# Kernel tuning notes

Hardware: AMD Instinct MI355X
Metric: run time of the kernel (lower is better)

Reference implementation:

```python
import jax, jax.numpy as jnp
import numpy as np

NUM_QUBITS = 22
NUM_LAYERS = 4
DIM = 2 ** NUM_QUBITS


def _apply_1q(state, U, q):
    # state: flat [2^n]; apply 2x2 unitary U on wire q (wire 0 = most significant)
    s = state.reshape(2 ** q, 2, -1)
    return jnp.einsum('ab,ibj->iaj', U, s).reshape(-1)


def _apply_cnot_adj(state, q):
    # CNOT with control q, target q+1 (adjacent wires)
    s = state.reshape(2 ** q, 2, 2, -1)
    s = jnp.stack([s[:, 0], s[:, 1, ::-1]], axis=1)
    return s.reshape(-1)


def _rot_mats(theta_x, theta_y, theta_z):
    cx = jnp.cos(theta_x / 2).astype(jnp.complex64)
    sx = jnp.sin(theta_x / 2).astype(jnp.complex64)
    RX = jnp.stack([jnp.stack([cx, -1j * sx]), jnp.stack([-1j * sx, cx])])
    cy = jnp.cos(theta_y / 2).astype(jnp.complex64)
    sy = jnp.sin(theta_y / 2).astype(jnp.complex64)
    RY = jnp.stack([jnp.stack([cy, -sy]), jnp.stack([sy, cy])])
    tz = theta_z.astype(jnp.complex64)
    zero = jnp.zeros((), jnp.complex64)
    RZ = jnp.stack([jnp.stack([jnp.exp(-1j * tz / 2), zero]),
                    jnp.stack([zero, jnp.exp(1j * tz / 2)])])
    return RX, RY, RZ


def _circuit(params, state):
    for l in range(NUM_LAYERS):
        for q in range(NUM_QUBITS):
            RX, RY, RZ = _rot_mats(params[l, q, 0], params[l, q, 1], params[l, q, 2])
            state = _apply_1q(state, RX, q)
            state = _apply_1q(state, RY, q)
            state = _apply_1q(state, RZ, q)
        for q in range(NUM_QUBITS - 1):
            state = _apply_cnot_adj(state, q)
    # <Z_q> for each qubit
    probs = jnp.abs(state) ** 2
    expvals = []
    for q in range(NUM_QUBITS):
        p = probs.reshape(2 ** q, 2, -1)
        expvals.append(p[:, 0].sum() - p[:, 1].sum())
    return jnp.stack(expvals).astype(jnp.float32)


def setup_inputs() -> dict:
    key = jax.random.key(0)
    k1, k2, k3 = jax.random.split(key, 3)
    params = jax.random.normal(k1, (NUM_LAYERS, NUM_QUBITS, 3), dtype=jnp.float32)
    state_re = jax.random.normal(k2, (DIM,), dtype=jnp.float32)
    state_im = jax.random.normal(k3, (DIM,), dtype=jnp.float32)
    return {"params": params, "state_re": state_re, "state_im": state_im}


def reference(params, state_re, state_im):
    state = (state_re + 1j * state_im).astype(jnp.complex64)
    state = state / jnp.sqrt(jnp.sum(jnp.abs(state) ** 2))
    return _circuit(params, state)
```

## Files before the change

kernel.cpp:

```cpp
#include <hip/hip_runtime.h>
#include <math.h>

#define NQ 22
#define DIM (1u << NQ)

typedef float v2f __attribute__((ext_vector_type(2)));

__global__ void k_gates(const float* __restrict__ params, float* __restrict__ U) {
  int t = blockIdx.x * blockDim.x + threadIdx.x;
  if (t >= 88) return;
  const float* p = params + t * 3;
  double hx = 0.5 * (double)p[0], hy = 0.5 * (double)p[1], hz = 0.5 * (double)p[2];
  double cx = cos(hx), sx = sin(hx);
  double cy = cos(hy), sy = sin(hy);
  double cz = cos(hz), sz = sin(hz);
  double m00r = cy * cx, m00i = sy * sx;
  double m01r = -sy * cx, m01i = -cy * sx;
  double m10r = sy * cx, m10i = -cy * sx;
  double m11r = cy * cx, m11i = -sy * sx;
  float* o = U + t * 8;
  o[0] = (float)(cz * m00r + sz * m00i); o[1] = (float)(cz * m00i - sz * m00r);
  o[2] = (float)(cz * m01r + sz * m01i); o[3] = (float)(cz * m01i - sz * m01r);
  o[4] = (float)(cz * m10r - sz * m10i); o[5] = (float)(cz * m10i + sz * m10r);
  o[6] = (float)(cz * m11r - sz * m11i); o[7] = (float)(cz * m11i + sz * m11r);
}

template <int NP>
__device__ __forceinline__ void apply_bit0(v2f RE[NP], v2f IM[NP], const float* __restrict__ u) {
  float u0 = u[0], u1 = u[1], u2 = u[2], u3 = u[3], u4 = u[4], u5 = u[5], u6 = u[6], u7 = u[7];
#pragma unroll
  for (int k = 0; k < NP; ++k) {
    float a0r = RE[k].x, a0i = IM[k].x, a1r = RE[k].y, a1i = IM[k].y;
    float n0r = u0 * a0r - u1 * a0i + u2 * a1r - u3 * a1i;
    float n0i = u0 * a0i + u1 * a0r + u2 * a1i + u3 * a1r;
    float n1r = u4 * a0r - u5 * a0i + u6 * a1r - u7 * a1i;
    float n1i = u4 * a0i + u5 * a0r + u6 * a1i + u7 * a1r;
    RE[k].x = n0r; IM[k].x = n0i; RE[k].y = n1r; IM[k].y = n1i;
  }
}

template <int NP, int PB>
__device__ __forceinline__ void apply_bitP(v2f RE[NP], v2f IM[NP], const float* __restrict__ u) {
  float u0 = u[0], u1 = u[1], u2 = u[2], u3 = u[3], u4 = u[4], u5 = u[5], u6 = u[6], u7 = u[7];
#pragma unroll
  for (int m = 0; m < NP / 2; ++m) {
    int k0 = ((m >> PB) << (PB + 1)) | (m & ((1 << PB) - 1));
    int k1 = k0 | (1 << PB);
    v2f a0r = RE[k0], a0i = IM[k0], a1r = RE[k1], a1i = IM[k1];
    v2f n0r = u0 * a0r - u1 * a0i + u2 * a1r - u3 * a1i;
    v2f n0i = u0 * a0i + u1 * a0r + u2 * a1i + u3 * a1r;
    v2f n1r = u4 * a0r - u5 * a0i + u6 * a1r - u7 * a1i;
    v2f n1i = u4 * a0i + u5 * a0r + u6 * a1i + u7 * a1r;
    RE[k0] = n0r; IM[k0] = n0i; RE[k1] = n1r; IM[k1] = n1i;
  }
}

__device__ __forceinline__ void apply4p(v2f RE[8], v2f IM[8], const float* __restrict__ U,
                                        int l, int wtop) {
  const float* base = U + ((l * 22 + wtop) << 3);
  apply_bit0<8>(RE, IM, base);
  apply_bitP<8, 0>(RE, IM, base - 8);
  apply_bitP<8, 1>(RE, IM, base - 16);
  apply_bitP<8, 2>(RE, IM, base - 24);
}

__device__ __forceinline__ void apply5p(v2f RE[16], v2f IM[16], const float* __restrict__ U,
                                        int l, int wtop) {
  const float* base = U + ((l * 22 + wtop) << 3);
  apply_bit0<16>(RE, IM, base);
  apply_bitP<16, 0>(RE, IM, base - 8);
  apply_bitP<16, 1>(RE, IM, base - 16);
  apply_bitP<16, 2>(RE, IM, base - 24);
  apply_bitP<16, 3>(RE, IM, base - 32);
}

template <typename WI, typename RI>
__device__ __forceinline__ void xchgP(float2* lds2, v2f RE[8], v2f IM[8], WI wi, RI ri) {
  __syncthreads();
#pragma unroll
  for (int d = 0; d < 16; ++d) {
    float2 a;
    if (d & 1) a = make_float2(RE[d >> 1].y, IM[d >> 1].y);
    else       a = make_float2(RE[d >> 1].x, IM[d >> 1].x);
    lds2[wi(d)] = a;
  }
  __syncthreads();
#pragma unroll
  for (int d = 0; d < 16; ++d) {
    float2 a = lds2[ri(d)];
    if (d & 1) { RE[d >> 1].y = a.x; IM[d >> 1].y = a.y; }
    else       { RE[d >> 1].x = a.x; IM[d >> 1].x = a.y; }
  }
}

__global__ __launch_bounds__(256, 4) void k_passA(const float* __restrict__ srcRe,
                                                  const float* __restrict__ srcIm,
                                                  const float2* __restrict__ src2,
                                                  float2* __restrict__ dst,
                                                  const float* __restrict__ U,
                                                  int layer, int first) {
  __shared__ float2 lds2[4096];
  const int t = threadIdx.x;
  const unsigned base = ((unsigned)blockIdx.x << 12) | ((unsigned)t << 4);
  v2f RE[8], IM[8];
  if (first) {
    const float4* r4 = (const float4*)(srcRe + base);
    const float4* i4 = (const float4*)(srcIm + base);
#pragma unroll
    for (int k = 0; k < 4; ++k) {
      float4 r = r4[k], m = i4[k];
      RE[2 * k].x     = r.x; RE[2 * k].y     = r.y;
      IM[2 * k].x     = m.x; IM[2 * k].y     = m.y;
      RE[2 * k + 1].x = r.z; RE[2 * k + 1].y = r.w;
      IM[2 * k + 1].x = m.z; IM[2 * k + 1].y = m.w;
    }
  } else {
    const unsigned b = base >> 4;
    const unsigned W = (b ^ (b >> 1)) << 4;
    const float4* s4 = (const float4*)(src2 + W);
    v2f WR[8], WI[8];
#pragma unroll
    for (int k = 0; k < 8; ++k) {
      float4 x = s4[k];
      WR[k].x = x.x; WR[k].y = x.z;
      WI[k].x = x.y; WI[k].y = x.w;
    }
    if (b & 1) {
#pragma unroll
      for (int k = 0; k < 4; ++k) {
        v2f tr = WR[k]; WR[k] = WR[k + 4]; WR[k + 4] = tr;
        v2f ti = WI[k]; WI[k] = WI[k + 4]; WI[k + 4] = ti;
      }
    }
#pragma unroll
    for (int k = 0; k < 8; ++k) {
      const int s = (2 * k) ^ k;
      const int j = s >> 1;
      if (s & 1) {
        RE[k].x = WR[j].y; RE[k].y = WR[j].x;
        IM[k].x = WI[j].y; IM[k].y = WI[j].x;
      } else {
        RE[k] = WR[j]; IM[k] = WI[j];
      }
    }
  }
  auto wA = [&](int d) { unsigned j = ((unsigned)t << 4) | (unsigned)d; return (int)(j ^ (j >> 4)); };
  auto rB = [&](int d) { unsigned j = (((unsigned)t >> 4) << 8) | ((unsigned)d << 4) | ((unsigned)t & 15); return (int)(j ^ (j >> 4)); };
  auto rC = [&](int d) { unsigned j = ((unsigned)d << 8) | (unsigned)t; return (int)(j ^ (j >> 4)); };

  apply4p(RE, IM, U, layer, 21);
  xchgP(lds2, RE, IM, wA, rB);
  apply4p(RE, IM, U, layer, 17);
  xchgP(lds2, RE, IM, rB, rC);
  apply4p(RE, IM, U, layer, 13);
  xchgP(lds2, RE, IM, rC, wA);
  float4* o4 = (float4*)(dst + base);
#pragma unroll
  for (int k = 0; k < 8; ++k)
    o4[k] = make_float4(RE[k].x, IM[k].x, RE[k].y, IM[k].y);
}

__device__ __forceinline__ int pb_lds_idx(unsigned h, unsigned c) {
  unsigned e = (h << 4) | (c ^ ((h ^ (h >> 5)) & 15u));
  return (int)(e ^ (((h >> 5) & 1u) << 4));
}

__global__ __launch_bounds__(512, 2) void k_passB(const float2* __restrict__ src,
                                                  float2* __restrict__ dst,
                                                  const float* __restrict__ U,
                                                  int layer) {
  __shared__ float lds[16384];
  const int t = threadIdx.x;
  const unsigned c = (unsigned)(t & 15), u = (unsigned)(t >> 4);
  const unsigned lowbase = ((unsigned)blockIdx.x << 4) | c;
  v2f RE[16], IM[16];
#pragma unroll
  for (int d = 0; d < 32; ++d) {
    unsigned h = u | ((unsigned)d << 5);
    float2 a = src[(h << 12) | lowbase];
    if (d & 1) { RE[d >> 1].y = a.x; IM[d >> 1].y = a.y; }
    else       { RE[d >> 1].x = a.x; IM[d >> 1].x = a.y; }
  }
  apply5p(RE, IM, U, layer, 4);
  __syncthreads();
#pragma unroll
  for (int d = 0; d < 32; ++d) {
    unsigned h = u | ((unsigned)d << 5);
    lds[pb_lds_idx(h, c)] = (d & 1) ? RE[d >> 1].y : RE[d >> 1].x;
  }
  __syncthreads();
#pragma unroll
  for (int d = 0; d < 32; ++d) {
    unsigned h = (unsigned)d | (u << 5);
    float a = lds[pb_lds_idx(h, c)];
    if (d & 1) RE[d >> 1].y = a; else RE[d >> 1].x = a;
  }
  __syncthreads();
#pragma unroll
  for (int d = 0; d < 32; ++d) {
    unsigned h = u | ((unsigned)d << 5);
    lds[pb_lds_idx(h, c)] = (d & 1) ? IM[d >> 1].y : IM[d >> 1].x;
  }
  __syncthreads();
#pragma unroll
  for (int d = 0; d < 32; ++d) {
    unsigned h = (unsigned)d | (u << 5);
    float a = lds[pb_lds_idx(h, c)];
    if (d & 1) IM[d >> 1].y = a; else IM[d >> 1].x = a;
  }
  apply5p(RE, IM, U, layer, 9);
#pragma unroll
  for (int d = 0; d < 32; ++d) {
    unsigned h = (unsigned)d | (u << 5);
    float2 a;
    if (d & 1) a = make_float2(RE[d >> 1].y, IM[d >> 1].y);
    else       a = make_float2(RE[d >> 1].x, IM[d >> 1].x);
    dst[(h << 12) | lowbase] = a;
  }
}

__global__ __launch_bounds__(512, 2) void k_passB_ev(const float2* __restrict__ src,
                                                     const float* __restrict__ U,
                                                     float* __restrict__ partials,
                                                     int layer) {
  __shared__ float lds[16384];
  const int t = threadIdx.x;
  const unsigned c = (unsigned)(t & 15), u = (unsigned)(t >> 4);
  const unsigned blk = blockIdx.x;
  const unsigned lowbase = (blk << 4) | c;
  v2f RE[16], IM[16];
#pragma unroll
  for (int d = 0; d < 32; ++d) {
    unsigned h = u | ((unsigned)d << 5);
    float2 a = src[(h << 12) | lowbase];
    if (d & 1) { RE[d >> 1].y = a.x; IM[d >> 1].y = a.y; }
    else       { RE[d >> 1].x = a.x; IM[d >> 1].x = a.y; }
  }
  apply5p(RE, IM, U, layer, 4);
  __syncthreads();
#pragma unroll
  for (int d = 0; d < 32; ++d) {
    unsigned h = u | ((unsigned)d << 5);
    lds[pb_lds_idx(h, c)] = (d & 1) ? RE[d >> 1].y : RE[d >> 1].x;
  }
  __syncthreads();
#pragma unroll
  for (int d = 0; d < 32; ++d) {
    unsigned h = (unsigned)d | (u << 5);
    float a = lds[pb_lds_idx(h, c)];
    if (d & 1) RE[d >> 1].y = a; else RE[d >> 1].x = a;
  }
  __syncthreads();
#pragma unroll
  for (int d = 0; d < 32; ++d) {
    unsigned h = u | ((unsigned)d << 5);
    lds[pb_lds_idx(h, c)] = (d & 1) ? IM[d >> 1].y : IM[d >> 1].x;
  }
  __syncthreads();
#pragma unroll
  for (int d = 0; d < 32; ++d) {
    unsigned h = (unsigned)d | (u << 5);
    float a = lds[pb_lds_idx(h, c)];
    if (d & 1) IM[d >> 1].y = a; else IM[d >> 1].x = a;
  }
  apply5p(RE, IM, U, layer, 9);

  v2f PS[16];
#pragma unroll
  for (int k = 0; k < 16; ++k) PS[k] = RE[k] * RE[k] + IM[k] * IM[k];
  v2f S4[8], B4[8];
#pragma unroll
  for (int k = 0; k < 8; ++k) { S4[k] = PS[k] + PS[k + 8]; B4[k] = PS[k] - PS[k + 8]; }
  float Tot = 0.f, W4 = 0.f;
#pragma unroll
  for (int k = 0; k < 8; ++k) { Tot += S4[k].x + S4[k].y; W4 += B4[k].x + B4[k].y; }
  v2f B3[4];
#pragma unroll
  for (int k = 0; k < 4; ++k) B3[k] = B4[k] - B4[k + 4];
  float W3 = (B3[0].x + B3[0].y) + (B3[1].x + B3[1].y) + (B3[2].x + B3[2].y) + (B3[3].x + B3[3].y);
  v2f B2[2];
  B2[0] = B3[0] - B3[2]; B2[1] = B3[1] - B3[3];
  float W2 = (B2[0].x + B2[0].y) + (B2[1].x + B2[1].y);
  v2f B1 = B2[0] - B2[1];
  float W1 = B1.x + B1.y;
  float W0 = B1.x - B1.y;

  unsigned y = lowbase; y ^= y >> 1; y ^= y >> 2; y ^= y >> 4; y ^= y >> 8;
  unsigned pu = (unsigned)__popc(u) & 1u;
  float acc[22];
#pragma unroll
  for (int q = 0; q <= 4; ++q)
    acc[q] = ((unsigned)__popc(u >> (4 - q)) & 1u) ? -Tot : Tot;
  {
    float W[5] = {W0, W1, W2, W3, W4};
#pragma unroll
    for (int q = 5; q <= 9; ++q)
      acc[q] = pu ? -W[9 - q] : W[9 - q];
  }
#pragma unroll
  for (int q = 10; q <= 21; ++q)
    acc[q] = (((y >> (21 - q)) ^ pu) & 1u) ? -W0 : W0;

  __syncthreads();
  float* red = lds;
  const int lane = t & 63, wv = t >> 6;
#pragma unroll
  for (int q = 0; q < 22; ++q) {
    float s = acc[q];
    for (int off = 32; off > 0; off >>= 1) s += __shfl_down(s, off, 64);
    if (lane == 0) red[wv * 23 + q] = s;
  }
  {
    float s = Tot;
    for (int off = 32; off > 0; off >>= 1) s += __shfl_down(s, off, 64);
    if (lane == 0) red[wv * 23 + 22] = s;
  }
  __syncthreads();
  if (t < 23) {
    float s = 0.f;
#pragma unroll
    for (int w = 0; w < 8; ++w) s += red[w * 23 + t];
    partials[t * 256 + blk] = s;
  }
}

__global__ void k_final(const float* __restrict__ partials, float* __restrict__ out) {
  __shared__ double res[32];
  const int t = threadIdx.x;
  const int r = t >> 3, l8 = t & 7;
  if (r < 23) {
    double s = 0.0;
    const float* p = partials + r * 256 + l8 * 32;
    for (int k = 0; k < 32; ++k) s += (double)p[k];
    for (int off = 4; off > 0; off >>= 1) s += __shfl_down(s, off, 8);
    if (l8 == 0) res[r] = s;
  }
  __syncthreads();
  if (t < 22) out[t] = (float)(res[t] / res[22]);
}

extern "C" void kernel_launch(void* const* d_in, const int* in_sizes, int n_in,
                              void* d_out, int out_size, void* d_ws, size_t ws_size,
                              hipStream_t stream) {
  const float* params = (const float*)d_in[0];
  const float* sre = (const float*)d_in[1];
  const float* sim = (const float*)d_in[2];
  float* out = (float*)d_out;
  char* ws = (char*)d_ws;
  float* U = (float*)ws;
  float* partials = (float*)(ws + 4096);
  float2* buf0 = (float2*)(ws + 131072);
  float2* buf1 = buf0 + DIM;

  k_gates<<<1, 128, 0, stream>>>(params, U);
  k_passA<<<1024, 256, 0, stream>>>(sre, sim, nullptr, buf0, U, 0, 1);
  k_passB<<<256, 512, 0, stream>>>(buf0, buf1, U, 0);
  for (int l = 1; l < 3; ++l) {
    k_passA<<<1024, 256, 0, stream>>>(nullptr, nullptr, buf1, buf0, U, l, 0);
    k_passB<<<256, 512, 0, stream>>>(buf0, buf1, U, l);
  }
  k_passA<<<1024, 256, 0, stream>>>(nullptr, nullptr, buf1, buf0, U, 3, 0);
  k_passB_ev<<<256, 512, 0, stream>>>(buf0, U, partials, 3);
  k_final<<<1, 256, 0, stream>>>(partials, out);
}
```

Before: 235.1 us.

## Shrink passB blocks to 256 threads, batch strided loads, new LDS swizzle

Pass B now uses 256-thread blocks, each covering 8 low-index columns instead of 16. The grid doubles to 512 blocks and the LDS tile halves, and the LDS swizzle function changes to match. All 32 strided global loads are issued into a temporary array before unpacking, in both pass B and pass A, so more memory requests are in flight at once. The partial-sum layout and the final reduction are resized for 512 blocks. The catch is that each wave now reads 8 contiguous float2s (64 bytes) per row rather than 128 bytes, which may reduce coalescing efficiency.

```diff
diff --git a/kernel.cpp b/kernel.cpp
--- a/kernel.cpp
+++ b/kernel.cpp
@@ -118,18 +118,20 @@
     const unsigned b = base >> 4;
     const unsigned W = (b ^ (b >> 1)) << 4;
     const float4* s4 = (const float4*)(src2 + W);
-    v2f WR[8], WI[8];
+    float4 raw[8];
+#pragma unroll
+    for (int k = 0; k < 8; ++k) raw[k] = s4[k];
+    v2f WR[8], WIm[8];
 #pragma unroll
     for (int k = 0; k < 8; ++k) {
-      float4 x = s4[k];
-      WR[k].x = x.x; WR[k].y = x.z;
-      WI[k].x = x.y; WI[k].y = x.w;
+      WR[k].x = raw[k].x; WR[k].y = raw[k].z;
+      WIm[k].x = raw[k].y; WIm[k].y = raw[k].w;
     }
     if (b & 1) {
 #pragma unroll
       for (int k = 0; k < 4; ++k) {
         v2f tr = WR[k]; WR[k] = WR[k + 4]; WR[k + 4] = tr;
-        v2f ti = WI[k]; WI[k] = WI[k + 4]; WI[k + 4] = ti;
+        v2f ti = WIm[k]; WIm[k] = WIm[k + 4]; WIm[k + 4] = ti;
       }
     }
 #pragma unroll
@@ -138,9 +140,9 @@
       const int j = s >> 1;
       if (s & 1) {
         RE[k].x = WR[j].y; RE[k].y = WR[j].x;
-        IM[k].x = WI[j].y; IM[k].y = WI[j].x;
+        IM[k].x = WIm[j].y; IM[k].y = WIm[j].x;
       } else {
-        RE[k] = WR[j]; IM[k] = WI[j];
+        RE[k] = WR[j]; IM[k] = WIm[j];
       }
     }
   }
@@ -160,52 +162,56 @@
     o4[k] = make_float4(RE[k].x, IM[k].x, RE[k].y, IM[k].y);
 }
 
-__device__ __forceinline__ int pb_lds_idx(unsigned h, unsigned c) {
-  unsigned e = (h << 4) | (c ^ ((h ^ (h >> 5)) & 15u));
-  return (int)(e ^ (((h >> 5) & 1u) << 4));
-}
-
-__global__ __launch_bounds__(512, 2) void k_passB(const float2* __restrict__ src,
+__device__ __forceinline__ int pb_idx(unsigned h, unsigned c) {
+  return (int)(((h << 3) | c) ^ (((h >> 5) & 3u) << 3));
+}
+
+__global__ __launch_bounds__(256, 2) void k_passB(const float2* __restrict__ src,
                                                   float2* __restrict__ dst,
                                                   const float* __restrict__ U,
                                                   int layer) {
-  __shared__ float lds[16384];
+  __shared__ float lds[8192];
   const int t = threadIdx.x;
-  const unsigned c = (unsigned)(t & 15), u = (unsigned)(t >> 4);
-  const unsigned lowbase = ((unsigned)blockIdx.x << 4) | c;
+  const unsigned c = (unsigned)(t & 7), u = (unsigned)(t >> 3);
+  const unsigned lowbase = ((unsigned)blockIdx.x << 3) | c;
+  const float2* sp = src + lowbase;
+  float2 tmp[32];
+#pragma unroll
+  for (int d = 0; d < 32; ++d) {
+    unsigned h = u | ((unsigned)d << 5);
+    tmp[d] = sp[(size_t)h << 12];
+  }
   v2f RE[16], IM[16];
 #pragma unroll
   for (int d = 0; d < 32; ++d) {
-    unsigned h = u | ((unsigned)d << 5);
-    float2 a = src[(h << 12) | lowbase];
-    if (d & 1) { RE[d >> 1].y = a.x; IM[d >> 1].y = a.y; }
-    else       { RE[d >> 1].x = a.x; IM[d >> 1].x = a.y; }
+    if (d & 1) { RE[d >> 1].y = tmp[d].x; IM[d >> 1].y = tmp[d].y; }
+    else       { RE[d >> 1].x = tmp[d].x; IM[d >> 1].x = tmp[d].y; }
   }
   apply5p(RE, IM, U, layer, 4);
   __syncthreads();
 #pragma unroll
   for (int d = 0; d < 32; ++d) {
     unsigned h = u | ((unsigned)d << 5);
-    lds[pb_lds_idx(h, c)] = (d & 1) ? RE[d >> 1].y : RE[d >> 1].x;
-  }
-  __syncthreads();
-#pragma unroll
-  for (int d = 0; d < 32; ++d) {
-    unsigned h = (unsigned)d | (u << 5);
-    float a = lds[pb_lds_idx(h, c)];
+    lds[pb_idx(h, c)] = (d & 1) ? RE[d >> 1].y : RE[d >> 1].x;
+  }
+  __syncthreads();
+#pragma unroll
+  for (int d = 0; d < 32; ++d) {
+    unsigned h = (unsigned)d | (u << 5);
+    float a = lds[pb_idx(h, c)];
     if (d & 1) RE[d >> 1].y = a; else RE[d >> 1].x = a;
   }
   __syncthreads();
 #pragma unroll
   for (int d = 0; d < 32; ++d) {
     unsigned h = u | ((unsigned)d << 5);
-    lds[pb_lds_idx(h, c)] = (d & 1) ? IM[d >> 1].y : IM[d >> 1].x;
-  }
-  __syncthreads();
-#pragma unroll
-  for (int d = 0; d < 32; ++d) {
-    unsigned h = (unsigned)d | (u << 5);
-    float a = lds[pb_lds_idx(h, c)];
+    lds[pb_idx(h, c)] = (d & 1) ? IM[d >> 1].y : IM[d >> 1].x;
+  }
+  __syncthreads();
+#pragma unroll
+  for (int d = 0; d < 32; ++d) {
+    unsigned h = (unsigned)d | (u << 5);
+    float a = lds[pb_idx(h, c)];
     if (d & 1) IM[d >> 1].y = a; else IM[d >> 1].x = a;
   }
   apply5p(RE, IM, U, layer, 9);
@@ -215,52 +221,57 @@
     float2 a;
     if (d & 1) a = make_float2(RE[d >> 1].y, IM[d >> 1].y);
     else       a = make_float2(RE[d >> 1].x, IM[d >> 1].x);
-    dst[(h << 12) | lowbase] = a;
-  }
-}
-
-__global__ __launch_bounds__(512, 2) void k_passB_ev(const float2* __restrict__ src,
+    dst[((size_t)h << 12) | lowbase] = a;
+  }
+}
+
+__global__ __launch_bounds__(256, 2) void k_passB_ev(const float2* __restrict__ src,
                                                      const float* __restrict__ U,
                                                      float* __restrict__ partials,
                                                      int layer) {
-  __shared__ float lds[16384];
+  __shared__ float lds[8192];
   const int t = threadIdx.x;
-  const unsigned c = (unsigned)(t & 15), u = (unsigned)(t >> 4);
+  const unsigned c = (unsigned)(t & 7), u = (unsigned)(t >> 3);
   const unsigned blk = blockIdx.x;
-  const unsigned lowbase = (blk << 4) | c;
+  const unsigned lowbase = (blk << 3) | c;
+  const float2* sp = src + lowbase;
+  float2 tmp[32];
+#pragma unroll
+  for (int d = 0; d < 32; ++d) {
+    unsigned h = u | ((unsigned)d << 5);
+    tmp[d] = sp[(size_t)h << 12];
+  }
   v2f RE[16], IM[16];
 #pragma unroll
   for (int d = 0; d < 32; ++d) {
-    unsigned h = u | ((unsigned)d << 5);
-    float2 a = src[(h << 12) | lowbase];
-    if (d & 1) { RE[d >> 1].y = a.x; IM[d >> 1].y = a.y; }
-    else       { RE[d >> 1].x = a.x; IM[d >> 1].x = a.y; }
+    if (d & 1) { RE[d >> 1].y = tmp[d].x; IM[d >> 1].y = tmp[d].y; }
+    else       { RE[d >> 1].x = tmp[d].x; IM[d >> 1].x = tmp[d].y; }
   }
   apply5p(RE, IM, U, layer, 4);
   __syncthreads();
 #pragma unroll
   for (int d = 0; d < 32; ++d) {
     unsigned h = u | ((unsigned)d << 5);
-    lds[pb_lds_idx(h, c)] = (d & 1) ? RE[d >> 1].y : RE[d >> 1].x;
-  }
-  __syncthreads();
-#pragma unroll
-  for (int d = 0; d < 32; ++d) {
-    unsigned h = (unsigned)d | (u << 5);
-    float a = lds[pb_lds_idx(h, c)];
+    lds[pb_idx(h, c)] = (d & 1) ? RE[d >> 1].y : RE[d >> 1].x;
+  }
+  __syncthreads();
+#pragma unroll
+  for (int d = 0; d < 32; ++d) {
+    unsigned h = (unsigned)d | (u << 5);
+    float a = lds[pb_idx(h, c)];
     if (d & 1) RE[d >> 1].y = a; else RE[d >> 1].x = a;
   }
   __syncthreads();
 #pragma unroll
   for (int d = 0; d < 32; ++d) {
     unsigned h = u | ((unsigned)d << 5);
-    lds[pb_lds_idx(h, c)] = (d & 1) ? IM[d >> 1].y : IM[d >> 1].x;
-  }
-  __syncthreads();
-#pragma unroll
-  for (int d = 0; d < 32; ++d) {
-    unsigned h = (unsigned)d | (u << 5);
-    float a = lds[pb_lds_idx(h, c)];
+    lds[pb_idx(h, c)] = (d & 1) ? IM[d >> 1].y : IM[d >> 1].x;
+  }
+  __syncthreads();
+#pragma unroll
+  for (int d = 0; d < 32; ++d) {
+    unsigned h = (unsigned)d | (u << 5);
+    float a = lds[pb_idx(h, c)];
     if (d & 1) IM[d >> 1].y = a; else IM[d >> 1].x = a;
   }
   apply5p(RE, IM, U, layer, 9);
@@ -319,8 +330,8 @@
   if (t < 23) {
     float s = 0.f;
 #pragma unroll
-    for (int w = 0; w < 8; ++w) s += red[w * 23 + t];
-    partials[t * 256 + blk] = s;
+    for (int w = 0; w < 4; ++w) s += red[w * 23 + t];
+    partials[t * 512 + blk] = s;
   }
 }
 
@@ -330,8 +341,8 @@
   const int r = t >> 3, l8 = t & 7;
   if (r < 23) {
     double s = 0.0;
-    const float* p = partials + r * 256 + l8 * 32;
-    for (int k = 0; k < 32; ++k) s += (double)p[k];
+    const float* p = partials + r * 512 + l8 * 64;
+    for (int k = 0; k < 64; ++k) s += (double)p[k];
     for (int off = 4; off > 0; off >>= 1) s += __shfl_down(s, off, 8);
     if (l8 == 0) res[r] = s;
   }
@@ -354,12 +365,12 @@
 
   k_gates<<<1, 128, 0, stream>>>(params, U);
   k_passA<<<1024, 256, 0, stream>>>(sre, sim, nullptr, buf0, U, 0, 1);
-  k_passB<<<256, 512, 0, stream>>>(buf0, buf1, U, 0);
+  k_passB<<<512, 256, 0, stream>>>(buf0, buf1, U, 0);
   for (int l = 1; l < 3; ++l) {
     k_passA<<<1024, 256, 0, stream>>>(nullptr, nullptr, buf1, buf0, U, l, 0);
-    k_passB<<<256, 512, 0, stream>>>(buf0, buf1, U, l);
+    k_passB<<<512, 256, 0, stream>>>(buf0, buf1, U, l);
   }
   k_passA<<<1024, 256, 0, stream>>>(nullptr, nullptr, buf1, buf0, U, 3, 0);
-  k_passB_ev<<<256, 512, 0, stream>>>(buf0, U, partials, 3);
+  k_passB_ev<<<512, 256, 0, stream>>>(buf0, U, partials, 3);
   k_final<<<1, 256, 0, stream>>>(partials, out);
 }
```

Measured after the change: 242.2 us. +3.0%, slower.
